# Kernel optimization log

Hardware: AMD Instinct MI355X
Metric: run time of the kernel (lower is better)

Reference implementation:

```python
import jax, jax.numpy as jnp
import numpy as np

INPUT_DIM = 1024
HIDDEN = 1024
NUM_EXPERTS = 64
TOP_K = 8
N_TOKENS = 32768


def _linear_params(key, fan_in, fan_out):
    kw, kb = jax.random.split(key)
    bound = 1.0 / np.sqrt(fan_in)
    w = jax.random.uniform(kw, (fan_in, fan_out), jnp.float32, -bound, bound)
    b = jax.random.uniform(kb, (fan_out,), jnp.float32, -bound, bound)
    return w, b


def setup_inputs() -> dict:
    key = jax.random.key(0)
    ks = jax.random.split(key, 8)
    x = jax.random.normal(ks[0], (N_TOKENS, INPUT_DIM), jnp.float32)
    noise = jax.random.normal(ks[1], (N_TOKENS, NUM_EXPERTS), jnp.float32)
    h2 = 2 * HIDDEN
    w1, b1 = _linear_params(ks[2], INPUT_DIM, h2)
    w2, b2 = _linear_params(ks[3], h2, h2)
    wn, bn = _linear_params(ks[4], h2, h2)
    w3, b3 = _linear_params(ks[5], h2, HIDDEN)
    w4, b4 = _linear_params(ks[6], HIDDEN, NUM_EXPERTS)
    wz, bz = _linear_params(ks[7], INPUT_DIM, NUM_EXPERTS)
    return {"x": x, "noise": noise, "w1": w1, "b1": b1, "w2": w2, "b2": b2,
            "wn": wn, "bn": bn, "w3": w3, "b3": b3, "w4": w4, "b4": b4,
            "wz": wz, "bz": bz}


def reference(x, noise, w1, b1, w2, b2, wn, bn, w3, b3, w4, b4, wz, bz):
    relu = jax.nn.relu
    h = relu(x @ w1 + b1)            # [N, 2H]
    h = relu(h @ w2 + b2)            # [N, 2H]
    h = relu(h @ wn + bn)            # [N, 2H]
    h = relu(h @ w3 + b3)            # [N, H]
    logits = h @ w4 + b4             # [N, E]
    noise_logits = x @ wz + bz       # [N, E]
    noisy_logits = logits + noise * jax.nn.softplus(noise_logits)
    top_k_logits, indices = jax.lax.top_k(noisy_logits, TOP_K)  # [N, K]
    rows = jnp.arange(noisy_logits.shape[0])[:, None]
    sparse_logits = jnp.full_like(noisy_logits, -jnp.inf).at[rows, indices].set(top_k_logits)
    router_output = jax.nn.softmax(sparse_logits, axis=-1)      # [N, E]
    return router_output, indices
```

## Files before the change

### kernel.cpp

```cpp
#include <hip/hip_runtime.h>
#include <math.h>

#define IN_DIM 1024
#define H2     2048
#define HID    1024
#define NEXP   64
#define TOPK   8
#define RISK_TH 1.5e-4f

typedef short  v8s __attribute__((ext_vector_type(8)));
typedef float  v4f __attribute__((ext_vector_type(4)));

__device__ __forceinline__ void bf16_split(float f, ushort& h, ushort& l) {
    unsigned uh = __float_as_uint(f) & 0xffff0000u;
    h = (ushort)(uh >> 16);
    float r = f - __uint_as_float(uh);
    l = (ushort)(__float_as_uint(r) >> 16);
}

__device__ __forceinline__ void gload16(const ushort* g, ushort* l) {
    __builtin_amdgcn_global_load_lds(
        (const __attribute__((address_space(1))) void*)g,
        (__attribute__((address_space(3))) void*)l, 16, 0, 0);
}

__global__ __launch_bounds__(256)
void split_w_kernel(const float* __restrict__ W, ushort* __restrict__ hiT,
                    ushort* __restrict__ loT, int K, int N)
{
    __shared__ float T[64][65];
    const int k0 = blockIdx.y * 64, n0 = blockIdx.x * 64;
    const int t = threadIdx.x;
#pragma unroll
    for (int j = 0; j < 4; ++j) {
        int idx = t + j * 256;
        int row = idx >> 4;
        int c4  = (idx & 15) * 4;
        float4 f = *(const float4*)(W + (long)(k0 + row) * N + n0 + c4);
        T[row][c4 + 0] = f.x; T[row][c4 + 1] = f.y;
        T[row][c4 + 2] = f.z; T[row][c4 + 3] = f.w;
    }
    __syncthreads();
#pragma unroll
    for (int j = 0; j < 4; ++j) {
        int idx = t + j * 256;
        int nn = idx >> 4;
        int kq = (idx & 15) * 4;
        ushort4 h4, l4;
        bf16_split(T[kq + 0][nn], h4.x, l4.x);
        bf16_split(T[kq + 1][nn], h4.y, l4.y);
        bf16_split(T[kq + 2][nn], h4.z, l4.z);
        bf16_split(T[kq + 3][nn], h4.w, l4.w);
        long o = (long)(n0 + nn) * K + k0 + kq;
        *(ushort4*)(hiT + o) = h4;
        *(ushort4*)(loT + o) = l4;
    }
}

__global__ __launch_bounds__(256)
void split_x_kernel(const float* __restrict__ X, ushort* __restrict__ hi,
                    ushort* __restrict__ lo)
{
    long i = ((long)blockIdx.x * 256 + threadIdx.x) * 4;
    float4 f = *(const float4*)(X + i);
    ushort4 h4, l4;
    bf16_split(f.x, h4.x, l4.x);
    bf16_split(f.y, h4.y, l4.y);
    bf16_split(f.z, h4.z, l4.z);
    bf16_split(f.w, h4.w, l4.w);
    *(ushort4*)(hi + i) = h4;
    *(ushort4*)(lo + i) = l4;
}

template<int MI, int NWN>
__global__ __launch_bounds__(512, 2)
void gemm8p_kernel(const ushort* __restrict__ gAhi, const ushort* __restrict__ gAlo,
                   const ushort* __restrict__ gBhi, const ushort* __restrict__ gBlo,
                   const float* __restrict__ bias,
                   float* __restrict__ Cf32, ushort* __restrict__ Chi,
                   ushort* __restrict__ Clo, int N, int K)
{
    static_assert(MI == 2 * NWN, "wave grid must tile 256 rows");
    constexpr int BN    = NWN * 64;
    constexpr int ATILE = 256 * 32;
    constexpr int BTILE = BN * 32;
    constexpr int BUFU  = 2 * ATILE + 2 * BTILE;
    constexpr int MH    = MI / 2;
    __shared__ __align__(16) ushort lds[2 * BUFU];

    const int tid  = threadIdx.x;
    const int w    = tid >> 6;
    const int lane = tid & 63;
    const int wm   = w / NWN;
    const int wn   = w % NWN;
    const int q    = lane >> 4;
    const int l15  = lane & 15;

    const int nwg = (int)(gridDim.x * gridDim.y);
    const int h   = (int)(blockIdx.y * gridDim.x + blockIdx.x);
    const int l   = (h & 7) * (nwg >> 3) + (h >> 3);
    const long bm = (long)(l >> 3) * 256;
    const long bn = (long)(l & 7) * BN;

    const int  e   = lane >> 2;
    const int  s8  = (((lane & 3) ^ ((lane >> 3) & 3)) * 8);
    const int  fragUS = ((q ^ ((l15 >> 1) & 3)) * 8);

    const int NT = K >> 5;

    auto stageA = [&](int ktv, ushort* nb) {
        const long gr = bm + w * 16 + e;
        gload16(gAhi + gr * K + ktv + s8,         nb + w * 512);
        gload16(gAhi + (gr + 128) * K + ktv + s8, nb + 128 * 32 + w * 512);
        gload16(gAlo + gr * K + ktv + s8,         nb + ATILE + w * 512);
        gload16(gAlo + (gr + 128) * K + ktv + s8, nb + ATILE + 128 * 32 + w * 512);
    };
    auto stageB = [&](int ktv, ushort* nb) {
        const long gr = bn + w * 16 + e;
        gload16(gBhi + gr * K + ktv + s8,         nb + 2 * ATILE + w * 512);
        gload16(gBlo + gr * K + ktv + s8,         nb + 2 * ATILE + BTILE + w * 512);
        if constexpr (BN == 256) {
            gload16(gBhi + (gr + 128) * K + ktv + s8, nb + 2 * ATILE + 128 * 32 + w * 512);
            gload16(gBlo + (gr + 128) * K + ktv + s8, nb + 2 * ATILE + BTILE + 128 * 32 + w * 512);
        }
    };

    v4f acc[MI][4];
#pragma unroll
    for (int mi = 0; mi < MI; ++mi)
#pragma unroll
        for (int ni = 0; ni < 4; ++ni)
            acc[mi][ni] = (v4f){0.f, 0.f, 0.f, 0.f};

    stageA(0, lds);
    stageB(0, lds);
    if (NT > 1) {
        stageA(32, lds + BUFU);
        stageB(32, lds + BUFU);
        if constexpr (BN == 256) asm volatile("s_waitcnt vmcnt(8)" ::: "memory");
        else                     asm volatile("s_waitcnt vmcnt(6)" ::: "memory");
    } else {
        asm volatile("s_waitcnt vmcnt(0)" ::: "memory");
    }
    __builtin_amdgcn_s_barrier();
    __builtin_amdgcn_sched_barrier(0);

    for (int t = 0; t < NT; ++t) {
        const ushort* cA = lds + (t & 1) * BUFU;
        const ushort* cB = cA + 2 * ATILE;
        ushort* rb = lds + (t & 1) * BUFU;
        const bool issue2 = (t + 2 < NT);
        const int  kt2 = (t + 2) << 5;

        v8s ah[MH], al[MH];
        v8s bh0[2], bl0[2];
        v8s bh1[2], bl1[2];

#pragma unroll
        for (int i = 0; i < MH; ++i) {
            int r = wm * (MI * 16) + i * 16 + l15;
            const ushort* pA = cA + r * 32 + fragUS;
            ah[i] = *(const v8s*)pA;
            al[i] = *(const v8s*)(pA + ATILE);
        }
#pragma unroll
        for (int j = 0; j < 2; ++j) {
            int r = wn * 64 + j * 16 + l15;
            const ushort* pB = cB + r * 32 + fragUS;
            bh0[j] = *(const v8s*)pB;
            bl0[j] = *(const v8s*)(pB + BTILE);
        }
#pragma unroll
        for (int j = 0; j < 2; ++j) {
            int r = wn * 64 + (2 + j) * 16 + l15;
            const ushort* pB = cB + r * 32 + fragUS;
            bh1[j] = *(const v8s*)pB;
            bl1[j] = *(const v8s*)(pB + BTILE);
        }

        __builtin_amdgcn_s_setprio(1);
#pragma unroll
        for (int i = 0; i < MH; ++i)
#pragma unroll
            for (int j = 0; j < 2; ++j) {
                v4f c = acc[i][j];
                c = __builtin_amdgcn_mfma_f32_16x16x32_bf16(al[i], bh0[j], c, 0, 0, 0);
                c = __builtin_amdgcn_mfma_f32_16x16x32_bf16(ah[i], bl0[j], c, 0, 0, 0);
                c = __builtin_amdgcn_mfma_f32_16x16x32_bf16(ah[i], bh0[j], c, 0, 0, 0);
                acc[i][j] = c;
            }
        __builtin_amdgcn_s_setprio(0);

        __builtin_amdgcn_s_setprio(1);
#pragma unroll
        for (int i = 0; i < MH; ++i)
#pragma unroll
            for (int j = 0; j < 2; ++j) {
                v4f c = acc[i][2 + j];
                c = __builtin_amdgcn_mfma_f32_16x16x32_bf16(al[i], bh1[j], c, 0, 0, 0);
                c = __builtin_amdgcn_mfma_f32_16x16x32_bf16(ah[i], bl1[j], c, 0, 0, 0);
                c = __builtin_amdgcn_mfma_f32_16x16x32_bf16(ah[i], bh1[j], c, 0, 0, 0);
                acc[i][2 + j] = c;
            }
        __builtin_amdgcn_s_setprio(0);

#pragma unroll
        for (int i = 0; i < MH; ++i) {
            int r = wm * (MI * 16) + (MH + i) * 16 + l15;
            const ushort* pA = cA + r * 32 + fragUS;
            ah[i] = *(const v8s*)pA;
            al[i] = *(const v8s*)(pA + ATILE);
        }
        asm volatile("s_waitcnt lgkmcnt(0)" ::: "memory");
        __builtin_amdgcn_sched_barrier(0);
        __builtin_amdgcn_s_barrier();
        __builtin_amdgcn_sched_barrier(0);
        if (issue2) {
            stageA(kt2, rb);
            stageB(kt2, rb);
        }
        __builtin_amdgcn_sched_barrier(0);

        __builtin_amdgcn_s_setprio(1);
#pragma unroll
        for (int i = 0; i < MH; ++i)
#pragma unroll
            for (int j = 0; j < 2; ++j) {
                v4f c = acc[MH + i][2 + j];
                c = __builtin_amdgcn_mfma_f32_16x16x32_bf16(al[i], bh1[j], c, 0, 0, 0);
                c = __builtin_amdgcn_mfma_f32_16x16x32_bf16(ah[i], bl1[j], c, 0, 0, 0);
                c = __builtin_amdgcn_mfma_f32_16x16x32_bf16(ah[i], bh1[j], c, 0, 0, 0);
                acc[MH + i][2 + j] = c;
            }
#pragma unroll
        for (int i = 0; i < MH; ++i)
#pragma unroll
            for (int j = 0; j < 2; ++j) {
                v4f c = acc[MH + i][j];
                c = __builtin_amdgcn_mfma_f32_16x16x32_bf16(al[i], bh0[j], c, 0, 0, 0);
                c = __builtin_amdgcn_mfma_f32_16x16x32_bf16(ah[i], bl0[j], c, 0, 0, 0);
                c = __builtin_amdgcn_mfma_f32_16x16x32_bf16(ah[i], bh0[j], c, 0, 0, 0);
                acc[MH + i][j] = c;
            }
        __builtin_amdgcn_s_setprio(0);

        if (t + 1 < NT) {
            if (issue2) {
                if constexpr (BN == 256) asm volatile("s_waitcnt vmcnt(8)" ::: "memory");
                else                     asm volatile("s_waitcnt vmcnt(6)" ::: "memory");
            } else {
                asm volatile("s_waitcnt vmcnt(0)" ::: "memory");
            }
            __builtin_amdgcn_sched_barrier(0);
            __builtin_amdgcn_s_barrier();
            __builtin_amdgcn_sched_barrier(0);
        }
    }

#pragma unroll
    for (int ni = 0; ni < 4; ++ni) {
        int col = (int)(bn + wn * 64 + ni * 16 + l15);
        float bv = bias[col];
#pragma unroll
        for (int mi = 0; mi < MI; ++mi) {
            long row0 = bm + wm * (MI * 16) + mi * 16 + q * 4;
#pragma unroll
            for (int r = 0; r < 4; ++r) {
                float v = fmaxf(acc[mi][ni][r] + bv, 0.f);
                long o = (row0 + r) * (long)N + col;
                if (Cf32) {
                    Cf32[o] = v;
                } else {
                    ushort hh, ll;
                    bf16_split(v, hh, ll);
                    Chi[o] = hh;
                    Clo[o] = ll;
                }
            }
        }
    }
}

#define SBM 64
#define SBK 32
#define SLDA 68

__global__ __launch_bounds__(256, 2)
void small_gemm_kernel(const float* __restrict__ A, const float* __restrict__ B,
                       const float* __restrict__ bias, float* __restrict__ C,
                       int K)
{
    __shared__ __align__(16) float Hs[SBK][SLDA];
    __shared__ __align__(16) float Ws[SBK][NEXP];
    const int tid = threadIdx.x;
    const int tx = tid & 15;
    const int ty = tid >> 4;
    const long bm = (long)blockIdx.x * SBM;
    const float* Ab = A + bm * K;

    float acc[4][4];
#pragma unroll
    for (int i = 0; i < 4; ++i)
#pragma unroll
        for (int j = 0; j < 4; ++j) acc[i][j] = 0.f;

    float4 aR[2], bR[2];
#pragma unroll
    for (int j = 0; j < 2; ++j) {
        int idx = tid + (j << 8);
        int ar = idx >> 3, ac = (idx & 7) << 2;
        aR[j] = *(const float4*)(Ab + (long)ar * K + ac);
        int br = idx >> 4, bc = (idx & 15) << 2;
        bR[j] = *(const float4*)(B + (long)br * NEXP + bc);
    }

    int kt = 0;
    for (;;) {
#pragma unroll
        for (int j = 0; j < 2; ++j) {
            int idx = tid + (j << 8);
            int ar = idx >> 3, ac = (idx & 7) << 2;
            Hs[ac + 0][ar] = aR[j].x;
            Hs[ac + 1][ar] = aR[j].y;
            Hs[ac + 2][ar] = aR[j].z;
            Hs[ac + 3][ar] = aR[j].w;
            int br = idx >> 4, bc = (idx & 15) << 2;
            *(float4*)&Ws[br][bc] = bR[j];
        }
        __syncthreads();

        kt += SBK;
        if (kt < K) {
#pragma unroll
            for (int j = 0; j < 2; ++j) {
                int idx = tid + (j << 8);
                int ar = idx >> 3, ac = (idx & 7) << 2;
                aR[j] = *(const float4*)(Ab + (long)ar * K + kt + ac);
                int br = idx >> 4, bc = (idx & 15) << 2;
                bR[j] = *(const float4*)(B + (long)(kt + br) * NEXP + bc);
            }
        }

#pragma unroll
        for (int k = 0; k < SBK; ++k) {
            float a[4], b[4];
            *(float4*)&a[0] = *(const float4*)&Hs[k][ty * 4];
            *(float4*)&b[0] = *(const float4*)&Ws[k][tx * 4];
#pragma unroll
            for (int i = 0; i < 4; ++i)
#pragma unroll
                for (int j = 0; j < 4; ++j)
                    acc[i][j] = fmaf(a[i], b[j], acc[i][j]);
        }
        __syncthreads();
        if (kt >= K) break;
    }

    float bv[4];
#pragma unroll
    for (int j = 0; j < 4; ++j) bv[j] = bias[tx * 4 + j];
#pragma unroll
    for (int i = 0; i < 4; ++i) {
        long row = bm + ty * 4 + i;
        float o[4];
#pragma unroll
        for (int j = 0; j < 4; ++j) o[j] = acc[i][j] + bv[j];
        *(float4*)(C + row * NEXP + tx * 4) = *(const float4*)&o[0];
    }
}

__global__ __launch_bounds__(256)
void router_kernel(const float* __restrict__ logits, const float* __restrict__ nlog,
                   const float* __restrict__ noise, float* __restrict__ rout,
                   float* __restrict__ idx_out, int rows, int rowBase,
                   int* __restrict__ ctrl, int* __restrict__ list, int maxr)
{
    const int wave = threadIdx.x >> 6;
    const int lane = threadIdx.x & 63;
    const long row = (long)blockIdx.x * 4 + wave;
    if (row >= rows) return;

    float lg = logits[row * NEXP + lane];
    float nl = nlog[row * NEXP + lane];
    float nz = noise[row * NEXP + lane];
    float sp = fmaxf(nl, 0.f) + log1pf(expf(-fabsf(nl)));
    float v  = lg + nz * sp;

    float orig = v;
    float work = v;
    bool  sel  = false;
    float myidx = 0.f;
    float m = 0.f, ssum = 0.f;
    float prev = 0.f, minGap = INFINITY;

#pragma unroll
    for (int r = 0; r < TOPK + 1; ++r) {
        float bvv = work;
        int   bi  = lane;
#pragma unroll
        for (int off = 32; off > 0; off >>= 1) {
            float ov = __shfl_xor(bvv, off);
            int   oi = __shfl_xor(bi, off);
            if (ov > bvv || (ov == bvv && oi < bi)) { bvv = ov; bi = oi; }
        }
        if (r > 0) minGap = fminf(minGap, prev - bvv);
        prev = bvv;
        if (r < TOPK) {
            if (r == 0) m = bvv;
            ssum += expf(bvv - m);
            if (lane == bi) { work = -INFINITY; sel = true; }
            if (lane == r)  myidx = (float)bi;
        }
    }

    float p = sel ? expf(orig - m) / ssum : 0.f;
    rout[row * NEXP + lane] = p;
    if (lane < TOPK) idx_out[row * TOPK + lane] = myidx;

    if (lane == 0 && minGap < RISK_TH) {
        int slot = atomicAdd(ctrl, 1);
        if (slot < maxr) list[slot] = rowBase + (int)row;
    }
}

__global__ void init_kernel(int* ctrl) { if (threadIdx.x == 0) ctrl[0] = 0; }

__global__ void pad_kernel(int* ctrl, int* list, int maxr)
{
    int cnt = ctrl[0]; if (cnt > maxr) cnt = maxr;
    int rounded = (cnt + 63) & ~63; if (rounded > maxr) rounded = maxr;
    if (threadIdx.x == 0) { ctrl[1] = rounded; ctrl[2] = cnt; }
    int fill = (cnt > 0) ? list[0] : 0;
    for (int i = cnt + threadIdx.x; i < rounded; i += blockDim.x) list[i] = fill;
}

__global__ __launch_bounds__(256)
void fixzero_kernel(double* P, const float* __restrict__ bias, int cols,
                    double* Z, int zcols, const int* __restrict__ ctrl)
{
    const int rp = blockIdx.y * 64;
    if (rp >= ctrl[1]) return;
    const int c0 = blockIdx.x * 64;
    if (P && c0 < cols) {
#pragma unroll
        for (int i = 0; i < 8; ++i) {
            int idx = threadIdx.x + i * 256;
            int row = idx >> 5;
            int col = (idx & 31) * 2;
            long o = (long)(rp + row) * cols + c0 + col;
            double2 v = *(double2*)(P + o);
            v.x = fmax(v.x + (double)bias[c0 + col],     0.0);
            v.y = fmax(v.y + (double)bias[c0 + col + 1], 0.0);
            *(double2*)(P + o) = v;
        }
    }
    if (Z && c0 < zcols) {
        const double2 z2 = {0.0, 0.0};
#pragma unroll
        for (int i = 0; i < 8; ++i) {
            int idx = threadIdx.x + i * 256;
            int row = idx >> 5;
            int col = (idx & 31) * 2;
            *(double2*)(Z + (long)(rp + row) * zcols + c0 + col) = z2;
        }
    }
}

#define DBM 64
#define DBN 64
#define DBK 32

__global__ __launch_bounds__(256)
void dgemm_ks(const double* __restrict__ A64, const float* __restrict__ A32,
              const int* __restrict__ rowList,
              const float* __restrict__ B, double* __restrict__ C,
              int N, int K, int kLen, const int* __restrict__ ctrl)
{
    const int mBase = blockIdx.y * DBM;
    if (mBase >= ctrl[1]) return;
    const int kBase = blockIdx.z * kLen;
    const int kEnd  = kBase + kLen;

    __shared__ __align__(16) double As[DBM][DBK + 2];
    __shared__ __align__(16) double Bs[DBK][DBN];
    __shared__ int rowIdx[DBM];

    const int tid = threadIdx.x;
    const int tx = tid & 15;
    const int ty = tid >> 4;
    const int nBase = blockIdx.x * DBN;

    if (A32 && tid < DBM) rowIdx[tid] = rowList[mBase + tid];
    __syncthreads();

    const int ar = tid >> 4;
    const int ak = (tid & 15) * 2;
    const int bc = (tid & 15) * 4;

    int rIdx[4];
    if (A32) {
#pragma unroll
        for (int j = 0; j < 4; ++j) rIdx[j] = rowIdx[ar + j * 16];
    }

    double acc[4][4];
#pragma unroll
    for (int i = 0; i < 4; ++i)
#pragma unroll
        for (int j = 0; j < 4; ++j) acc[i][j] = 0.0;

    double2 aReg[4];
    float4  bReg[2];

    auto prefetch = [&](int ktv) {
#pragma unroll
        for (int j = 0; j < 4; ++j) {
            if (A32) {
                const float2 f = *(const float2*)(A32 + (long)rIdx[j] * K + ktv + ak);
                aReg[j].x = (double)f.x; aReg[j].y = (double)f.y;
            } else {
                aReg[j] = *(const double2*)(A64 + (long)(mBase + ar + j * 16) * K + ktv + ak);
            }
        }
#pragma unroll
        for (int j = 0; j < 2; ++j)
            bReg[j] = *(const float4*)(B + (long)(ktv + ar + j * 16) * N + nBase + bc);
    };

    prefetch(kBase);
    int kt = kBase;
    for (;;) {
#pragma unroll
        for (int j = 0; j < 4; ++j)
            *(double2*)&As[ar + j * 16][ak] = aReg[j];
#pragma unroll
        for (int j = 0; j < 2; ++j) {
            double2 lo, hi;
            lo.x = (double)bReg[j].x; lo.y = (double)bReg[j].y;
            hi.x = (double)bReg[j].z; hi.y = (double)bReg[j].w;
            *(double2*)&Bs[ar + j * 16][bc]     = lo;
            *(double2*)&Bs[ar + j * 16][bc + 2] = hi;
        }
        __syncthreads();

        kt += DBK;
        if (kt < kEnd) prefetch(kt);

#pragma unroll
        for (int k = 0; k < DBK; ++k) {
            double a[4], b[4];
#pragma unroll
            for (int i = 0; i < 4; ++i) a[i] = As[ty * 4 + i][k];
#pragma unroll
            for (int j = 0; j < 4; ++j) b[j] = Bs[k][tx + j * 16];
#pragma unroll
            for (int i = 0; i < 4; ++i)
#pragma unroll
                for (int j = 0; j < 4; ++j)
                    acc[i][j] = fma(a[i], b[j], acc[i][j]);
        }
        __syncthreads();
        if (kt >= kEnd) break;
    }

#pragma unroll
    for (int i = 0; i < 4; ++i) {
        long row = mBase + ty * 4 + i;
#pragma unroll
        for (int j = 0; j < 4; ++j) {
            int n = nBase + tx + j * 16;
#if defined(__HIP_PLATFORM_AMD__)
            unsafeAtomicAdd(&C[row * N + n], acc[i][j]);
#else
            atomicAdd(&C[row * N + n], acc[i][j]);
#endif
        }
    }
}

__global__ __launch_bounds__(256)
void router_fix_kernel(const double* __restrict__ lgd, const double* __restrict__ nld,
                       const float* __restrict__ b4f, const float* __restrict__ bzf,
                       const float* __restrict__ noise, float* __restrict__ rout,
                       float* __restrict__ idx_out,
                       const int* __restrict__ ctrl, const int* __restrict__ list)
{
    const int wave = threadIdx.x >> 6;
    const int lane = threadIdx.x & 63;
    const int i = blockIdx.x * 4 + wave;
    if (i >= ctrl[2]) return;
    const long row = list[i];

    double lg = lgd[(long)i * NEXP + lane] + (double)b4f[lane];
    double nl = nld[(long)i * NEXP + lane] + (double)bzf[lane];
    double nz = (double)noise[row * NEXP + lane];
    double sp = fmax(nl, 0.0) + log1p(exp(-fabs(nl)));
    double v  = lg + nz * sp;

    double orig = v, work = v;
    bool sel = false;
    float myidx = 0.f;
    double m = 0.0, ssum = 0.0;

#pragma unroll
    for (int r = 0; r < TOPK; ++r) {
        double bvv = work;
        int    bi  = lane;
#pragma unroll
        for (int off = 32; off > 0; off >>= 1) {
            double ov = __shfl_xor(bvv, off);
            int    oi = __shfl_xor(bi, off);
            if (ov > bvv || (ov == bvv && oi < bi)) { bvv = ov; bi = oi; }
        }
        if (r == 0) m = bvv;
        ssum += exp(bvv - m);
        if (lane == bi) { work = -INFINITY; sel = true; }
        if (lane == r)  myidx = (float)bi;
    }

    double p = sel ? exp(orig - m) / ssum : 0.0;
    rout[row * NEXP + lane] = (float)p;
    if (lane < TOPK) idx_out[row * TOPK + lane] = myidx;
}

extern "C" void kernel_launch(void* const* d_in, const int* in_sizes, int n_in,
                              void* d_out, int out_size, void* d_ws, size_t ws_size,
                              hipStream_t stream)
{
    const float* x     = (const float*)d_in[0];
    const float* noise = (const float*)d_in[1];
    const float* w1 = (const float*)d_in[2];
    const float* b1 = (const float*)d_in[3];
    const float* w2 = (const float*)d_in[4];
    const float* b2 = (const float*)d_in[5];
    const float* wn = (const float*)d_in[6];
    const float* bn = (const float*)d_in[7];
    const float* w3 = (const float*)d_in[8];
    const float* b3 = (const float*)d_in[9];
    const float* w4 = (const float*)d_in[10];
    const float* b4 = (const float*)d_in[11];
    const float* wz = (const float*)d_in[12];
    const float* bz = (const float*)d_in[13];
    float* out = (float*)d_out;

    const int Ntok = in_sizes[0] / IN_DIM;

    const size_t e1 = (size_t)IN_DIM * H2;
    const size_t e2 = (size_t)H2 * H2;
    const size_t en = (size_t)H2 * H2;
    const size_t e3 = (size_t)H2 * HID;
    size_t weightBytes = 2 * (e1 + e2 + en + e3) * sizeof(ushort);
    weightBytes = (weightBytes + 255) & ~(size_t)255;

    const size_t perTok = (size_t)4 * H2 * 2 + (size_t)IN_DIM * 4 + 2 * NEXP * 4;
    int chunk = 8192;
    while (chunk > 256) {
        size_t needb = weightBytes + (size_t)chunk * perTok + 65536;
        if (needb <= ws_size) break;
        chunk >>= 1;
    }
    if (chunk > Ntok) chunk = Ntok;

    int MAXR = chunk / 2;
    if (MAXR > 4096) MAXR = 4096;

    ushort* w1Thi = (ushort*)d_ws;
    ushort* w1Tlo = w1Thi + e1;
    ushort* w2Thi = w1Tlo + e1;
    ushort* w2Tlo = w2Thi + e2;
    ushort* wnThi = w2Tlo + e2;
    ushort* wnTlo = wnThi + en;
    ushort* w3Thi = wnTlo + en;
    ushort* w3Tlo = w3Thi + e3;

    char* region = (char*)d_ws + weightBytes;
    const size_t regionBytes = (size_t)chunk * perTok;

    ushort* pAhi = (ushort*)region;
    ushort* pAlo = pAhi + (size_t)chunk * H2;
    ushort* pBhi = pAlo + (size_t)chunk * H2;
    ushort* pBlo = pBhi + (size_t)chunk * H2;
    char*   ureg = (char*)(pBlo + (size_t)chunk * H2);
    ushort* xphi = (ushort*)ureg;
    ushort* xplo = xphi + (size_t)chunk * IN_DIM;
    float*  hfin = (float*)ureg;
    float*  lg   = (float*)(ureg + (size_t)chunk * IN_DIM * 4);
    float*  nl   = lg + (size_t)chunk * NEXP;

    double* hA  = (double*)region;
    double* hB  = hA + (size_t)MAXR * H2;
    double* lgd = hB + (size_t)MAXR * H2;
    double* nld = lgd + (size_t)MAXR * NEXP;

    int* ctrl = (int*)(region + regionBytes);
    int* list = ctrl + 16;

    float* ridx = out + (size_t)Ntok * NEXP;

    const dim3 blk(256);
    init_kernel<<<1, 64, 0, stream>>>(ctrl);

    split_w_kernel<<<dim3(H2 / 64,  IN_DIM / 64), blk, 0, stream>>>(w1, w1Thi, w1Tlo, IN_DIM, H2);
    split_w_kernel<<<dim3(H2 / 64,  H2 / 64),     blk, 0, stream>>>(w2, w2Thi, w2Tlo, H2, H2);
    split_w_kernel<<<dim3(H2 / 64,  H2 / 64),     blk, 0, stream>>>(wn, wnThi, wnTlo, H2, H2);
    split_w_kernel<<<dim3(HID / 64, H2 / 64),     blk, 0, stream>>>(w3, w3Thi, w3Tlo, H2, HID);

    for (int c0 = 0; c0 < Ntok; c0 += chunk) {
        const float* xa = x + (size_t)c0 * IN_DIM;
        split_x_kernel<<<dim3(chunk), blk, 0, stream>>>(xa, xphi, xplo);
        gemm8p_kernel<8, 4><<<dim3(H2 / 256,  chunk / 256), 512, 0, stream>>>(
            xphi, xplo, w1Thi, w1Tlo, b1, nullptr, pAhi, pAlo, H2, IN_DIM);
        gemm8p_kernel<8, 4><<<dim3(H2 / 256,  chunk / 256), 512, 0, stream>>>(
            pAhi, pAlo, w2Thi, w2Tlo, b2, nullptr, pBhi, pBlo, H2, H2);
        gemm8p_kernel<8, 4><<<dim3(H2 / 256,  chunk / 256), 512, 0, stream>>>(
            pBhi, pBlo, wnThi, wnTlo, bn, nullptr, pAhi, pAlo, H2, H2);
        gemm8p_kernel<4, 2><<<dim3(HID / 128, chunk / 256), 512, 0, stream>>>(
            pAhi, pAlo, w3Thi, w3Tlo, b3, hfin, nullptr, nullptr, HID, H2);
        small_gemm_kernel<<<dim3(chunk / SBM), blk, 0, stream>>>(hfin, w4, b4, lg, HID);
        small_gemm_kernel<<<dim3(chunk / SBM), blk, 0, stream>>>(xa,   wz, bz, nl, IN_DIM);
        router_kernel<<<dim3(chunk / 4), blk, 0, stream>>>(lg, nl, noise + (size_t)c0 * NEXP,
                                                           out + (size_t)c0 * NEXP,
                                                           ridx + (size_t)c0 * TOPK, chunk, c0,
                                                           ctrl, list, MAXR);
    }

    pad_kernel<<<1, 256, 0, stream>>>(ctrl, list, MAXR);

    const int GY = MAXR / DBM;
    fixzero_kernel<<<dim3(H2 / 64, GY), blk, 0, stream>>>(nullptr, nullptr, 0, hA, H2, ctrl);
    dgemm_ks<<<dim3(H2 / DBN, GY, 8), blk, 0, stream>>>(nullptr, x, list, w1, hA, H2, IN_DIM, IN_DIM / 8, ctrl);
    fixzero_kernel<<<dim3(H2 / 64, GY), blk, 0, stream>>>(hA, b1, H2, hB, H2, ctrl);
    dgemm_ks<<<dim3(H2 / DBN, GY, 8), blk, 0, stream>>>(hA, nullptr, nullptr, w2, hB, H2, H2, H2 / 8, ctrl);
    fixzero_kernel<<<dim3(H2 / 64, GY), blk, 0, stream>>>(hB, b2, H2, hA, H2, ctrl);
    dgemm_ks<<<dim3(H2 / DBN, GY, 8), blk, 0, stream>>>(hB, nullptr, nullptr, wn, hA, H2, H2, H2 / 8, ctrl);
    fixzero_kernel<<<dim3(H2 / 64, GY), blk, 0, stream>>>(hA, bn, H2, hB, HID, ctrl);
    dgemm_ks<<<dim3(HID / DBN, GY, 8), blk, 0, stream>>>(hA, nullptr, nullptr, w3, hB, HID, H2, H2 / 8, ctrl);
    fixzero_kernel<<<dim3(HID / 64, GY), blk, 0, stream>>>(hB, b3, HID, lgd, NEXP, ctrl);
    fixzero_kernel<<<dim3(1, GY), blk, 0, stream>>>(nullptr, nullptr, 0, nld, NEXP, ctrl);
    dgemm_ks<<<dim3(1, GY, 16), blk, 0, stream>>>(hB, nullptr, nullptr, w4, lgd, NEXP, HID, HID / 16, ctrl);
    dgemm_ks<<<dim3(1, GY, 16), blk, 0, stream>>>(nullptr, x, list, wz, nld, NEXP, IN_DIM, IN_DIM / 16, ctrl);
    router_fix_kernel<<<dim3(MAXR / 4), blk, 0, stream>>>(lgd, nld, b4, bz, noise, out, ridx, ctrl, list);
}
```

Measured before the change: 3.167 ms.

## Switch GEMM to single-stage prefetch with interleaved MFMA and merge small GEMMs

The main bf16-split GEMM loop drops its two-deep prefetch (stage t+2 issued mid-iteration with partial vmcnt waits). It now issues the loads for stage t+1 right after the fragment reads and waits for all of them at the end of the iteration. The three MFMA passes per accumulator are interleaved across independent accumulators, which shortens dependent MFMA chains but leaves fewer loads in flight. The two small logit GEMMs are merged into one launch, using blockIdx.y to pick the operands. Because HID equals IN_DIM, a single K value serves both.

```diff
diff --git a/kernel.cpp b/kernel.cpp
--- a/kernel.cpp
+++ b/kernel.cpp
@@ -134,23 +134,16 @@
 
     stageA(0, lds);
     stageB(0, lds);
-    if (NT > 1) {
-        stageA(32, lds + BUFU);
-        stageB(32, lds + BUFU);
-        if constexpr (BN == 256) asm volatile("s_waitcnt vmcnt(8)" ::: "memory");
-        else                     asm volatile("s_waitcnt vmcnt(6)" ::: "memory");
-    } else {
-        asm volatile("s_waitcnt vmcnt(0)" ::: "memory");
-    }
+    asm volatile("s_waitcnt vmcnt(0)" ::: "memory");
     __builtin_amdgcn_s_barrier();
     __builtin_amdgcn_sched_barrier(0);
 
     for (int t = 0; t < NT; ++t) {
         const ushort* cA = lds + (t & 1) * BUFU;
         const ushort* cB = cA + 2 * ATILE;
-        ushort* rb = lds + (t & 1) * BUFU;
-        const bool issue2 = (t + 2 < NT);
-        const int  kt2 = (t + 2) << 5;
+        ushort* nb = lds + ((t + 1) & 1) * BUFU;
+        const bool more = (t + 1 < NT);
+        const int  ktn  = (t + 1) << 5;
 
         v8s ah[MH], al[MH];
         v8s bh0[2], bl0[2];
@@ -177,30 +170,32 @@
             bh1[j] = *(const v8s*)pB;
             bl1[j] = *(const v8s*)(pB + BTILE);
         }
+        if (more) {
+            stageA(ktn, nb);
+            stageB(ktn, nb);
+        }
 
         __builtin_amdgcn_s_setprio(1);
 #pragma unroll
         for (int i = 0; i < MH; ++i)
 #pragma unroll
             for (int j = 0; j < 2; ++j) {
-                v4f c = acc[i][j];
-                c = __builtin_amdgcn_mfma_f32_16x16x32_bf16(al[i], bh0[j], c, 0, 0, 0);
-                c = __builtin_amdgcn_mfma_f32_16x16x32_bf16(ah[i], bl0[j], c, 0, 0, 0);
-                c = __builtin_amdgcn_mfma_f32_16x16x32_bf16(ah[i], bh0[j], c, 0, 0, 0);
-                acc[i][j] = c;
-            }
-        __builtin_amdgcn_s_setprio(0);
-
-        __builtin_amdgcn_s_setprio(1);
+                acc[i][j]     = __builtin_amdgcn_mfma_f32_16x16x32_bf16(al[i], bh0[j], acc[i][j],     0, 0, 0);
+                acc[i][2 + j] = __builtin_amdgcn_mfma_f32_16x16x32_bf16(al[i], bh1[j], acc[i][2 + j], 0, 0, 0);
+            }
 #pragma unroll
         for (int i = 0; i < MH; ++i)
 #pragma unroll
             for (int j = 0; j < 2; ++j) {
-                v4f c = acc[i][2 + j];
-                c = __builtin_amdgcn_mfma_f32_16x16x32_bf16(al[i], bh1[j], c, 0, 0, 0);
-                c = __builtin_amdgcn_mfma_f32_16x16x32_bf16(ah[i], bl1[j], c, 0, 0, 0);
-                c = __builtin_amdgcn_mfma_f32_16x16x32_bf16(ah[i], bh1[j], c, 0, 0, 0);
-                acc[i][2 + j] = c;
+                acc[i][j]     = __builtin_amdgcn_mfma_f32_16x16x32_bf16(ah[i], bl0[j], acc[i][j],     0, 0, 0);
+                acc[i][2 + j] = __builtin_amdgcn_mfma_f32_16x16x32_bf16(ah[i], bl1[j], acc[i][2 + j], 0, 0, 0);
+            }
+#pragma unroll
+        for (int i = 0; i < MH; ++i)
+#pragma unroll
+            for (int j = 0; j < 2; ++j) {
+                acc[i][j]     = __builtin_amdgcn_mfma_f32_16x16x32_bf16(ah[i], bh0[j], acc[i][j],     0, 0, 0);
+                acc[i][2 + j] = __builtin_amdgcn_mfma_f32_16x16x32_bf16(ah[i], bh1[j], acc[i][2 + j], 0, 0, 0);
             }
         __builtin_amdgcn_s_setprio(0);
 
@@ -211,50 +206,34 @@
             ah[i] = *(const v8s*)pA;
             al[i] = *(const v8s*)(pA + ATILE);
         }
-        asm volatile("s_waitcnt lgkmcnt(0)" ::: "memory");
-        __builtin_amdgcn_sched_barrier(0);
+
+        __builtin_amdgcn_s_setprio(1);
+#pragma unroll
+        for (int i = 0; i < MH; ++i)
+#pragma unroll
+            for (int j = 0; j < 2; ++j) {
+                acc[MH + i][2 + j] = __builtin_amdgcn_mfma_f32_16x16x32_bf16(al[i], bh1[j], acc[MH + i][2 + j], 0, 0, 0);
+                acc[MH + i][j]     = __builtin_amdgcn_mfma_f32_16x16x32_bf16(al[i], bh0[j], acc[MH + i][j],     0, 0, 0);
+            }
+#pragma unroll
+        for (int i = 0; i < MH; ++i)
+#pragma unroll
+            for (int j = 0; j < 2; ++j) {
+                acc[MH + i][2 + j] = __builtin_amdgcn_mfma_f32_16x16x32_bf16(ah[i], bl1[j], acc[MH + i][2 + j], 0, 0, 0);
+                acc[MH + i][j]     = __builtin_amdgcn_mfma_f32_16x16x32_bf16(ah[i], bl0[j], acc[MH + i][j],     0, 0, 0);
+            }
+#pragma unroll
+        for (int i = 0; i < MH; ++i)
+#pragma unroll
+            for (int j = 0; j < 2; ++j) {
+                acc[MH + i][2 + j] = __builtin_amdgcn_mfma_f32_16x16x32_bf16(ah[i], bh1[j], acc[MH + i][2 + j], 0, 0, 0);
+                acc[MH + i][j]     = __builtin_amdgcn_mfma_f32_16x16x32_bf16(ah[i], bh0[j], acc[MH + i][j],     0, 0, 0);
+            }
+        __builtin_amdgcn_s_setprio(0);
+
+        asm volatile("s_waitcnt vmcnt(0)" ::: "memory");
         __builtin_amdgcn_s_barrier();
         __builtin_amdgcn_sched_barrier(0);
-        if (issue2) {
-            stageA(kt2, rb);
-            stageB(kt2, rb);
-        }
-        __builtin_amdgcn_sched_barrier(0);
-
-        __builtin_amdgcn_s_setprio(1);
-#pragma unroll
-        for (int i = 0; i < MH; ++i)
-#pragma unroll
-            for (int j = 0; j < 2; ++j) {
-                v4f c = acc[MH + i][2 + j];
-                c = __builtin_amdgcn_mfma_f32_16x16x32_bf16(al[i], bh1[j], c, 0, 0, 0);
-                c = __builtin_amdgcn_mfma_f32_16x16x32_bf16(ah[i], bl1[j], c, 0, 0, 0);
-                c = __builtin_amdgcn_mfma_f32_16x16x32_bf16(ah[i], bh1[j], c, 0, 0, 0);
-                acc[MH + i][2 + j] = c;
-            }
-#pragma unroll
-        for (int i = 0; i < MH; ++i)
-#pragma unroll
-            for (int j = 0; j < 2; ++j) {
-                v4f c = acc[MH + i][j];
-                c = __builtin_amdgcn_mfma_f32_16x16x32_bf16(al[i], bh0[j], c, 0, 0, 0);
-                c = __builtin_amdgcn_mfma_f32_16x16x32_bf16(ah[i], bl0[j], c, 0, 0, 0);
-                c = __builtin_amdgcn_mfma_f32_16x16x32_bf16(ah[i], bh0[j], c, 0, 0, 0);
-                acc[MH + i][j] = c;
-            }
-        __builtin_amdgcn_s_setprio(0);
-
-        if (t + 1 < NT) {
-            if (issue2) {
-                if constexpr (BN == 256) asm volatile("s_waitcnt vmcnt(8)" ::: "memory");
-                else                     asm volatile("s_waitcnt vmcnt(6)" ::: "memory");
-            } else {
-                asm volatile("s_waitcnt vmcnt(0)" ::: "memory");
-            }
-            __builtin_amdgcn_sched_barrier(0);
-            __builtin_amdgcn_s_barrier();
-            __builtin_amdgcn_sched_barrier(0);
-        }
     }
 
 #pragma unroll
@@ -286,10 +265,16 @@
 #define SLDA 68
 
 __global__ __launch_bounds__(256, 2)
-void small_gemm_kernel(const float* __restrict__ A, const float* __restrict__ B,
-                       const float* __restrict__ bias, float* __restrict__ C,
-                       int K)
-{
+void small_gemm2_kernel(const float* __restrict__ A0, const float* __restrict__ A1,
+                        const float* __restrict__ B0, const float* __restrict__ B1,
+                        const float* __restrict__ bias0, const float* __restrict__ bias1,
+                        float* __restrict__ C0, float* __restrict__ C1, int K)
+{
+    const float* A    = blockIdx.y ? A1 : A0;
+    const float* B    = blockIdx.y ? B1 : B0;
+    const float* bias = blockIdx.y ? bias1 : bias0;
+    float*       C    = blockIdx.y ? C1 : C0;
+
     __shared__ __align__(16) float Hs[SBK][SLDA];
     __shared__ __align__(16) float Ws[SBK][NEXP];
     const int tid = threadIdx.x;
@@ -716,8 +701,8 @@
             pBhi, pBlo, wnThi, wnTlo, bn, nullptr, pAhi, pAlo, H2, H2);
         gemm8p_kernel<4, 2><<<dim3(HID / 128, chunk / 256), 512, 0, stream>>>(
             pAhi, pAlo, w3Thi, w3Tlo, b3, hfin, nullptr, nullptr, HID, H2);
-        small_gemm_kernel<<<dim3(chunk / SBM), blk, 0, stream>>>(hfin, w4, b4, lg, HID);
-        small_gemm_kernel<<<dim3(chunk / SBM), blk, 0, stream>>>(xa,   wz, bz, nl, IN_DIM);
+        small_gemm2_kernel<<<dim3(chunk / SBM, 2), blk, 0, stream>>>(
+            hfin, xa, w4, wz, b4, bz, lg, nl, IN_DIM);
         router_kernel<<<dim3(chunk / 4), blk, 0, stream>>>(lg, nl, noise + (size_t)c0 * NEXP,
                                                            out + (size_t)c0 * NEXP,
                                                            ridx + (size_t)c0 * TOPK, chunk, c0,
```

After: 2.934 ms. 1.08x faster.
